# Optimization experiments

Hardware: AMD Instinct MI355X
Metric: run time of the kernel (lower is better)

## Reference

```python
import jax, jax.numpy as jnp
import numpy as np

EMB = 1024
FF = 4096
NE = 8
TOPK = 2
TEMP = 1.0


def setup_inputs() -> dict:
    key = jax.random.key(0)
    ks = jax.random.split(key, 8)
    s_emb = 1.0 / np.sqrt(EMB)
    s_ff = 1.0 / np.sqrt(FF)
    x = jax.random.normal(ks[0], (4, 2048, EMB), dtype=jnp.float32)
    gate_W = jax.random.uniform(ks[1], (EMB, NE), minval=-s_emb, maxval=s_emb, dtype=jnp.float32)
    gate_b = jax.random.uniform(ks[2], (NE,), minval=-s_emb, maxval=s_emb, dtype=jnp.float32)
    W1 = jax.random.uniform(ks[3], (NE, EMB, FF), minval=-s_emb, maxval=s_emb, dtype=jnp.float32)
    b1 = jax.random.uniform(ks[4], (NE, FF), minval=-s_emb, maxval=s_emb, dtype=jnp.float32)
    W2 = jax.random.uniform(ks[5], (NE, FF, EMB), minval=-s_ff, maxval=s_ff, dtype=jnp.float32)
    b2 = jax.random.uniform(ks[6], (NE, EMB), minval=-s_ff, maxval=s_ff, dtype=jnp.float32)
    return {"x": x, "gate_W": gate_W, "gate_b": gate_b, "W1": W1, "b1": b1, "W2": W2, "b2": b2}


def reference(x, gate_W, gate_b, W1, b1, W2, b2):
    B, S, D = x.shape
    xf = x.reshape(-1, D)  # [T, D]
    T = xf.shape[0]

    gate_logits = (xf @ gate_W + gate_b) / TEMP            # [T, E]
    gate_scores = jax.nn.softmax(gate_logits, axis=-1)     # [T, E]
    topk_scores, topk_idx = jax.lax.top_k(gate_scores, TOPK)
    topk_scores = topk_scores / jnp.sum(topk_scores, axis=-1, keepdims=True)

    # combine_weights[t, e] = sum_i topk_scores[t, i] * (topk_idx[t, i] == e)
    onehot = jax.nn.one_hot(topk_idx, NE, dtype=xf.dtype)  # [T, K, E]
    combine = jnp.einsum('tk,tke->te', topk_scores, onehot)  # [T, E]

    # Dense per-expert FFN (dropout is identity in eval): h = gelu(x W1 + b1); y = h W2 + b2
    h = jax.nn.gelu(jnp.einsum('td,edf->etf', xf, W1) + b1[:, None, :], approximate=False)
    y = jnp.einsum('etf,efd->etd', h, W2) + b2[:, None, :]  # [E, T, D]
    out = jnp.einsum('te,etd->td', combine, y).reshape(B, S, D)

    # Load-balance auxiliary loss
    expert_counts = jnp.sum(onehot, axis=(0, 1))            # [E]
    expert_fraction = expert_counts / (T * TOPK)
    routing_weights = jnp.mean(gate_scores, axis=0)
    aux_loss = NE * jnp.sum(expert_fraction * routing_weights)
    return out, aux_loss
```

## Files before the change

kernel.cpp:

```cpp
#include <hip/hip_runtime.h>
#include <math.h>

#define EMB 1024
#define FF  4096
#define NE  8
#define TTOK 8192

typedef __attribute__((ext_vector_type(4))) float  f32x4;
typedef __attribute__((ext_vector_type(8))) __bf16 bf16x8;

#define MAXROWS  18432

#define WS_COUNTS  0
#define WS_CURSORS 1024
#define WS_SSUM    1056
#define WS_NTILES  2080
#define WS_BASE    2084
#define WS_TILE_E  2176
#define WS_TILE_RB 2816
#define WS_TKIDX   4096
#define WS_TKW     69632
#define WS_SLOT    135168
#define WS_TOKID   200704
#define WS_ROWW    274432
#define WS_BIG2    350208

#define SZ_W1T ((size_t)NE * EMB * FF * 2)
#define SZ_W2T ((size_t)NE * EMB * FF * 2)
#define SZ_XB  ((size_t)TTOK * EMB * 2)
#define SZ_H   ((size_t)MAXROWS * FF * 2)
#define SZ_Y   ((size_t)MAXROWS * EMB * 4)

__device__ inline f32x4 fzero() { f32x4 v = {0.f, 0.f, 0.f, 0.f}; return v; }

__device__ __forceinline__ void gl16(const void* g, void* l) {
    __builtin_amdgcn_global_load_lds(
        (const __attribute__((address_space(1))) void*)g,
        (__attribute__((address_space(3))) void*)l, 16, 0, 0);
}

__device__ __forceinline__ float gelu_f(float v) {
    float u = fabsf(v) * 0.70710678118654752f;
    float p = 1.0f + u * (0.278393f + u * (0.230389f + u * (0.000972f + u * 0.078108f)));
    p = p * p; p = p * p;
    float er = 1.0f - 1.0f / p;
    float s = (v >= 0.0f) ? er : -er;
    return 0.5f * v * (1.0f + s);
}

__global__ __launch_bounds__(256) void gate_kernel(
    const float* __restrict__ x, const float* __restrict__ gW, const float* __restrict__ gb,
    int* counts, float* ssum, int* tk_idx, float* tk_w)
{
    int wave = threadIdx.x >> 6;
    int lane = threadIdx.x & 63;
    int t = blockIdx.x * 4 + wave;

    float acc[NE];
#pragma unroll
    for (int e = 0; e < NE; e++) acc[e] = 0.f;

    const float* xr = x + (size_t)t * EMB;
#pragma unroll
    for (int i = 0; i < 4; i++) {
        int d0 = i * 256 + lane * 4;
        f32x4 xv = *(const f32x4*)(xr + d0);
#pragma unroll
        for (int j = 0; j < 4; j++) {
            const float* wrow = gW + (size_t)(d0 + j) * NE;
            float xs = xv[j];
#pragma unroll
            for (int e = 0; e < NE; e++) acc[e] += xs * wrow[e];
        }
    }
#pragma unroll
    for (int e = 0; e < NE; e++) {
#pragma unroll
        for (int off = 32; off; off >>= 1) acc[e] += __shfl_xor(acc[e], off, 64);
    }
    if (lane == 0) {
        float sc[NE];
        float m = -1e30f;
        for (int e = 0; e < NE; e++) { sc[e] = acc[e] + gb[e]; m = fmaxf(m, sc[e]); }
        float sum = 0.f;
        for (int e = 0; e < NE; e++) { sc[e] = expf(sc[e] - m); sum += sc[e]; }
        float inv = 1.f / sum;
        for (int e = 0; e < NE; e++) sc[e] *= inv;
        int i0 = 0; float s0 = sc[0];
        for (int e = 1; e < NE; e++) if (sc[e] > s0) { s0 = sc[e]; i0 = e; }
        int i1 = -1; float s1 = -1e30f;
        for (int e = 0; e < NE; e++) if (e != i0 && sc[e] > s1) { s1 = sc[e]; i1 = e; }
        float rn = 1.f / (s0 + s1);
        tk_idx[2 * t]     = i0;  tk_idx[2 * t + 1] = i1;
        tk_w[2 * t]       = s0 * rn;  tk_w[2 * t + 1] = s1 * rn;
        int slot = blockIdx.x & 31;
        atomicAdd(&counts[i0 * 32 + slot], 1);
        atomicAdd(&counts[i1 * 32 + slot], 1);
        for (int e = 0; e < NE; e++) atomicAdd(&ssum[e * 32 + slot], sc[e]);
    }
}

__global__ void route_build_kernel(const int* counts, const float* ssum,
                                   int* ntiles, int* base, int* tile_e, int* tile_rb,
                                   float* out_aux)
{
    if (threadIdx.x != 0 || blockIdx.x != 0) return;
    int total = 0, tiles = 0;
    float aux = 0.f;
    for (int e = 0; e < NE; e++) {
        int c = 0; float ss = 0.f;
        for (int j = 0; j < 32; j++) { c += counts[e * 32 + j]; ss += ssum[e * 32 + j]; }
        base[e] = total;
        int nt = (c + 255) >> 8;
        for (int i = 0; i < nt; i++) { tile_e[tiles] = e; tile_rb[tiles] = total + (i << 8); tiles++; }
        total += nt << 8;
        aux += ((float)c / (float)(TTOK * 2)) * (ss / (float)TTOK);
    }
    *ntiles = tiles;
    *out_aux = aux * (float)NE;
}

__global__ __launch_bounds__(256) void scatter_kernel(
    const int* __restrict__ tk_idx, const float* __restrict__ tk_w,
    const int* __restrict__ base, int* cursors, int* token_id, float* roww,
    int* slot_of)
{
    int t = blockIdx.x * 256 + threadIdx.x;
#pragma unroll
    for (int k = 0; k < 2; k++) {
        int e = tk_idx[2 * t + k];
        int pos = atomicAdd(&cursors[e], 1);
        int slot = base[e] + pos;
        token_id[slot] = t;
        roww[slot] = tk_w[2 * t + k];
        slot_of[2 * t + k] = slot;
    }
}

__global__ __launch_bounds__(256) void combine_kernel(
    const float* __restrict__ y0, const float* __restrict__ y1, int nsplit,
    const int* __restrict__ slot_of,
    const int* __restrict__ tk_idx, const float* __restrict__ tk_w,
    const float* __restrict__ b2, float* __restrict__ out)
{
    int t = blockIdx.x;
    int dq = threadIdx.x * 4;
    int s0 = slot_of[2 * t], s1 = slot_of[2 * t + 1];
    int e0 = tk_idx[2 * t], e1 = tk_idx[2 * t + 1];
    float w0 = tk_w[2 * t], w1 = tk_w[2 * t + 1];
    f32x4 ya = *(const f32x4*)(y0 + (size_t)s0 * EMB + dq);
    f32x4 yb = *(const f32x4*)(y0 + (size_t)s1 * EMB + dq);
    if (nsplit == 2) {
        f32x4 za = *(const f32x4*)(y1 + (size_t)s0 * EMB + dq);
        f32x4 zb = *(const f32x4*)(y1 + (size_t)s1 * EMB + dq);
#pragma unroll
        for (int q = 0; q < 4; q++) { ya[q] += za[q]; yb[q] += zb[q]; }
    }
    f32x4 ba = *(const f32x4*)(b2 + (size_t)e0 * EMB + dq);
    f32x4 bb = *(const f32x4*)(b2 + (size_t)e1 * EMB + dq);
    f32x4 r;
#pragma unroll
    for (int q = 0; q < 4; q++) r[q] = w0 * (ya[q] + ba[q]) + w1 * (yb[q] + bb[q]);
    *(f32x4*)(out + (size_t)t * EMB + dq) = r;
}

__global__ __launch_bounds__(256) void cvt_x_kernel(const float* __restrict__ x, __bf16* __restrict__ xb)
{
    size_t i = ((size_t)blockIdx.x * 256 + threadIdx.x) * 8;
    f32x4 a = *(const f32x4*)(x + i);
    f32x4 b = *(const f32x4*)(x + i + 4);
    bf16x8 o;
#pragma unroll
    for (int q = 0; q < 4; q++) { o[q] = (__bf16)a[q]; o[q + 4] = (__bf16)b[q]; }
    *(bf16x8*)(xb + i) = o;
}

__global__ __launch_bounds__(256) void transpose_cvt_kernel(
    const float* __restrict__ in, __bf16* __restrict__ outb, int R, int C)
{
    int e = blockIdx.z;
    const float* src = in + (size_t)e * R * C;
    __bf16* dst = outb + (size_t)e * R * C;
    __shared__ __bf16 Ls[64 * 72];
    int t = threadIdx.x;
    int r0 = blockIdx.x * 64, c0 = blockIdx.y * 64;
    int ri = t >> 4, cj = (t & 15) * 4;
#pragma unroll
    for (int p = 0; p < 4; p++) {
        int r = ri + p * 16;
        f32x4 v = *(const f32x4*)(src + (size_t)(r0 + r) * C + c0 + cj);
#pragma unroll
        for (int q = 0; q < 4; q++) Ls[(cj + q) * 72 + r] = (__bf16)v[q];
    }
    __syncthreads();
    int c = t >> 2, rq = (t & 3) * 16;
    bf16x8 a = *(bf16x8*)&Ls[c * 72 + rq];
    bf16x8 b = *(bf16x8*)&Ls[c * 72 + rq + 8];
    *(bf16x8*)(dst + (size_t)(c0 + c) * R + r0 + rq) = a;
    *(bf16x8*)(dst + (size_t)(c0 + c) * R + r0 + rq + 8) = b;
}


__device__ __forceinline__ void read_frags(const __bf16* lds, const int* off, bf16x8* v, int n) {
#pragma unroll
    for (int i = 0; i < n; i++) v[i] = *(const bf16x8*)(lds + off[i]);
}

__global__ __launch_bounds__(512, 2) void gemm1_8p(
    const __bf16* __restrict__ xb, const __bf16* __restrict__ W1T,
    const float* __restrict__ b1,
    const int* __restrict__ token_id, const int* __restrict__ tile_e,
    const int* __restrict__ tile_rb, const int* __restrict__ ntiles,
    __bf16* __restrict__ h)
{
    extern __shared__ __bf16 lds[];
    int flat = blockIdx.x;
    int c8 = flat & 7, r = flat >> 3;
    int mti = r >> 4, nb = r & 15;
    int mt = c8 * 9 + mti;
    if (mt >= *ntiles) return;
    int e = tile_e[mt], rb = tile_rb[mt];
    int n0 = nb * 256;

    int tid = threadIdx.x, lane = tid & 63, wid = tid >> 6;
    int wr = wid >> 2, wc = wid & 3;
    int cl = lane & 15, cq = lane >> 4;

    int srow = tid >> 2;
    int schunk = (tid & 3) ^ ((tid >> 3) & 3);
    const __bf16* ag[2];
#pragma unroll
    for (int hm = 0; hm < 2; hm++) {
        int tok = token_id[rb + hm * 128 + srow];
        if (tok < 0) tok = 0;
        ag[hm] = xb + (size_t)tok * EMB + schunk * 8;
    }
    const __bf16* bg[2];
#pragma unroll
    for (int hn = 0; hn < 2; hn++)
        bg[hn] = W1T + ((size_t)e * FF + (size_t)(n0 + hn * 128 + srow)) * EMB + schunk * 8;

    int sdA0 = wid * 512, sdA1 = 4096 + wid * 512;
    int sdB0 = 8192 + wid * 512, sdB1 = 12288 + wid * 512;

    int xoffe = (cq ^ ((cl >> 1) & 3)) * 8;
    int aoff[8], boff[4];
#pragma unroll
    for (int mi = 0; mi < 8; mi++) {
        int rr = wr * 128 + mi * 16 + cl;
        aoff[mi] = (rr >> 7) * 4096 + (rr & 127) * 32 + xoffe;
    }
#pragma unroll
    for (int ni = 0; ni < 4; ni++) {
        int nn = wc * 64 + ni * 16 + cl;
        boff[ni] = 8192 + (nn >> 7) * 4096 + (nn & 127) * 32 + xoffe;
    }

    f32x4 acc[8][4];
#pragma unroll
    for (int i = 0; i < 8; i++)
#pragma unroll
        for (int j = 0; j < 4; j++) acc[i][j] = fzero();

    const int NT = EMB / 32;
#pragma unroll
    for (int t0 = 0; t0 < 2; t0++) {
        __bf16* bp = lds + t0 * 16384;
        int k0 = t0 * 32;
        gl16(ag[0] + k0, bp + sdA0);
        gl16(ag[1] + k0, bp + sdA1);
        gl16(bg[0] + k0, bp + sdB0);
        gl16(bg[1] + k0, bp + sdB1);
    }
    asm volatile("s_waitcnt vmcnt(4)" ::: "memory");
    __builtin_amdgcn_s_barrier();

    int cb = 0;
#pragma unroll 1
    for (int t = 0; t < NT; t++) {
        const __bf16* cp = lds + cb * 16384;
        int sb = cb + 2; if (sb >= 3) sb -= 3;
        __bf16* sp = lds + sb * 16384;
        int kt = t + 2;
        int ko = kt * 32;
        if (kt < NT) {
            gl16(ag[0] + ko, sp + sdA0);
            gl16(ag[1] + ko, sp + sdA1);
            gl16(bg[0] + ko, sp + sdB0);
            gl16(bg[1] + ko, sp + sdB1);
        }
        bf16x8 b[4], a[8];
        read_frags(cp, boff, b, 4);
        read_frags(cp, aoff, a, 8);
        __builtin_amdgcn_s_setprio(1);
#pragma unroll
        for (int mi = 0; mi < 8; mi++)
#pragma unroll
            for (int ni = 0; ni < 4; ni++)
                acc[mi][ni] = __builtin_amdgcn_mfma_f32_16x16x32_bf16(a[mi], b[ni], acc[mi][ni], 0, 0, 0);
        __builtin_amdgcn_s_setprio(0);
        if (t < NT - 2)       { asm volatile("s_waitcnt vmcnt(4)" ::: "memory"); }
        else if (t == NT - 2) { asm volatile("s_waitcnt vmcnt(0)" ::: "memory"); }
        __builtin_amdgcn_s_barrier();
        cb = cb + 1; if (cb >= 3) cb = 0;
    }

    const float* b1g = b1 + (size_t)e * FF + n0;
#pragma unroll
    for (int mi = 0; mi < 8; mi++) {
#pragma unroll
        for (int ni = 0; ni < 4; ni++) {
            int col = wc * 64 + ni * 16 + cl;
            float bias = b1g[col];
#pragma unroll
            for (int j = 0; j < 4; j++) {
                int row = wr * 128 + mi * 16 + cq * 4 + j;
                float v = acc[mi][ni][j] + bias;
                h[(size_t)(rb + row) * FF + n0 + col] = (__bf16)gelu_f(v);
            }
        }
    }
}

__global__ __launch_bounds__(512, 2) void gemm2_8p(
    const __bf16* __restrict__ h, const __bf16* __restrict__ W2T,
    const int* __restrict__ tile_e, const int* __restrict__ tile_rb,
    const int* __restrict__ ntiles,
    float* __restrict__ y0, float* __restrict__ y1, int nsplit)
{
    extern __shared__ __bf16 lds[];
    int flat = blockIdx.x;
    int c8 = flat & 7, r = flat >> 3;
    int z = r / 36; int r36 = r - z * 36;
    int mti = r36 >> 2, nb = r36 & 3;
    int mt = c8 * 9 + mti;
    if (mt >= *ntiles) return;
    int e = tile_e[mt], rb = tile_rb[mt];
    int n0 = nb * 256;
    int KC = FF / nsplit;
    int koff = z * KC;
    float* y = z ? y1 : y0;

    int tid = threadIdx.x, lane = tid & 63, wid = tid >> 6;
    int wr = wid >> 2, wc = wid & 3;
    int cl = lane & 15, cq = lane >> 4;

    int srow = tid >> 2;
    int schunk = (tid & 3) ^ ((tid >> 3) & 3);
    const __bf16* ag[2];
#pragma unroll
    for (int hm = 0; hm < 2; hm++)
        ag[hm] = h + (size_t)(rb + hm * 128 + srow) * FF + koff + schunk * 8;
    const __bf16* bg[2];
#pragma unroll
    for (int hn = 0; hn < 2; hn++)
        bg[hn] = W2T + ((size_t)e * EMB + (size_t)(n0 + hn * 128 + srow)) * FF + koff + schunk * 8;

    int sdA0 = wid * 512, sdA1 = 4096 + wid * 512;
    int sdB0 = 8192 + wid * 512, sdB1 = 12288 + wid * 512;

    int xoffe = (cq ^ ((cl >> 1) & 3)) * 8;
    int aoff[8], boff[4];
#pragma unroll
    for (int mi = 0; mi < 8; mi++) {
        int rr = wr * 128 + mi * 16 + cl;
        aoff[mi] = (rr >> 7) * 4096 + (rr & 127) * 32 + xoffe;
    }
#pragma unroll
    for (int ni = 0; ni < 4; ni++) {
        int nn = wc * 64 + ni * 16 + cl;
        boff[ni] = 8192 + (nn >> 7) * 4096 + (nn & 127) * 32 + xoffe;
    }

    f32x4 acc[8][4];
#pragma unroll
    for (int i = 0; i < 8; i++)
#pragma unroll
        for (int j = 0; j < 4; j++) acc[i][j] = fzero();

    const int NT = KC / 32;
#pragma unroll
    for (int t0 = 0; t0 < 2; t0++) {
        __bf16* bp = lds + t0 * 16384;
        int k0 = t0 * 32;
        gl16(ag[0] + k0, bp + sdA0);
        gl16(ag[1] + k0, bp + sdA1);
        gl16(bg[0] + k0, bp + sdB0);
        gl16(bg[1] + k0, bp + sdB1);
    }
    asm volatile("s_waitcnt vmcnt(4)" ::: "memory");
    __builtin_amdgcn_s_barrier();

    int cb = 0;
#pragma unroll 1
    for (int t = 0; t < NT; t++) {
        const __bf16* cp = lds + cb * 16384;
        int sb = cb + 2; if (sb >= 3) sb -= 3;
        __bf16* sp = lds + sb * 16384;
        int kt = t + 2;
        int ko = kt * 32;
        if (kt < NT) {
            gl16(ag[0] + ko, sp + sdA0);
            gl16(ag[1] + ko, sp + sdA1);
            gl16(bg[0] + ko, sp + sdB0);
            gl16(bg[1] + ko, sp + sdB1);
        }
        bf16x8 b[4], a[8];
        read_frags(cp, boff, b, 4);
        read_frags(cp, aoff, a, 8);
        __builtin_amdgcn_s_setprio(1);
#pragma unroll
        for (int mi = 0; mi < 8; mi++)
#pragma unroll
            for (int ni = 0; ni < 4; ni++)
                acc[mi][ni] = __builtin_amdgcn_mfma_f32_16x16x32_bf16(a[mi], b[ni], acc[mi][ni], 0, 0, 0);
        __builtin_amdgcn_s_setprio(0);
        if (t < NT - 2)       { asm volatile("s_waitcnt vmcnt(4)" ::: "memory"); }
        else if (t == NT - 2) { asm volatile("s_waitcnt vmcnt(0)" ::: "memory"); }
        __builtin_amdgcn_s_barrier();
        cb = cb + 1; if (cb >= 3) cb = 0;
    }

#pragma unroll
    for (int mi = 0; mi < 8; mi++) {
#pragma unroll
        for (int ni = 0; ni < 4; ni++) {
            int col = wc * 64 + ni * 16 + cl;
#pragma unroll
            for (int j = 0; j < 4; j++) {
                int row = wr * 128 + mi * 16 + cq * 4 + j;
                y[(size_t)(rb + row) * EMB + n0 + col] = acc[mi][ni][j];
            }
        }
    }
}

extern "C" void kernel_launch(void* const* d_in, const int* in_sizes, int n_in,
                              void* d_out, int out_size, void* d_ws, size_t ws_size,
                              hipStream_t stream)
{
    const float* x   = (const float*)d_in[0];
    const float* gW  = (const float*)d_in[1];
    const float* gb  = (const float*)d_in[2];
    const float* W1  = (const float*)d_in[3];
    const float* b1  = (const float*)d_in[4];
    const float* W2  = (const float*)d_in[5];
    const float* b2  = (const float*)d_in[6];
    float* out = (float*)d_out;

    char* ws = (char*)d_ws;
    int*   counts  = (int*)(ws + WS_COUNTS);
    int*   cursors = (int*)(ws + WS_CURSORS);
    float* ssum    = (float*)(ws + WS_SSUM);
    int*   ntiles  = (int*)(ws + WS_NTILES);
    int*   base    = (int*)(ws + WS_BASE);
    int*   tile_e  = (int*)(ws + WS_TILE_E);
    int*   tile_rb = (int*)(ws + WS_TILE_RB);
    int*   tk_idx  = (int*)(ws + WS_TKIDX);
    float* tk_w    = (float*)(ws + WS_TKW);
    int*   slot_of = (int*)(ws + WS_SLOT);
    int*   token_id= (int*)(ws + WS_TOKID);
    float* roww    = (float*)(ws + WS_ROWW);

    __bf16* W1T  = (__bf16*)(ws + WS_BIG2);
    __bf16* xb   = (__bf16*)(ws + WS_BIG2 + SZ_W1T);
    __bf16* W2T  = (__bf16*)(ws + WS_BIG2 + SZ_W1T + SZ_XB);
    __bf16* hbuf = (__bf16*)(ws + WS_BIG2 + SZ_W1T + SZ_XB + SZ_W2T);
    size_t fixedend = WS_BIG2 + SZ_W1T + SZ_XB + SZ_W2T;

    float* y0 = (float*)(ws + WS_BIG2);
    float* y1 = (float*)(ws + fixedend + SZ_H);
    int nsplit = (ws_size >= fixedend + SZ_H + SZ_Y) ? 2 : 1;

    hipFuncSetAttribute((const void*)gemm1_8p, hipFuncAttributeMaxDynamicSharedMemorySize, 98304);
    hipFuncSetAttribute((const void*)gemm2_8p, hipFuncAttributeMaxDynamicSharedMemorySize, 98304);

    hipMemsetAsync(ws + WS_COUNTS, 0, 2080, stream);
    hipMemsetAsync(ws + WS_TOKID, 0xFF, (size_t)MAXROWS * 4, stream);

    cvt_x_kernel<<<TTOK * EMB / 2048, 256, 0, stream>>>(x, xb);
    transpose_cvt_kernel<<<dim3(EMB / 64, FF / 64, NE), 256, 0, stream>>>(W1, W1T, EMB, FF);
    transpose_cvt_kernel<<<dim3(FF / 64, EMB / 64, NE), 256, 0, stream>>>(W2, W2T, FF, EMB);

    gate_kernel<<<TTOK / 4, 256, 0, stream>>>(x, gW, gb, counts, ssum, tk_idx, tk_w);
    route_build_kernel<<<1, 64, 0, stream>>>(counts, ssum, ntiles, base, tile_e, tile_rb,
                                             out + (size_t)TTOK * EMB);
    scatter_kernel<<<TTOK / 256, 256, 0, stream>>>(tk_idx, tk_w, base, cursors, token_id, roww, slot_of);

    gemm1_8p<<<8 * 9 * 16, 512, 98304, stream>>>(
        xb, W1T, b1, token_id, tile_e, tile_rb, ntiles, hbuf);
    gemm2_8p<<<8 * 9 * 4 * nsplit, 512, 98304, stream>>>(
        hbuf, W2T, tile_e, tile_rb, ntiles, y0, y1, nsplit);
    combine_kernel<<<TTOK, 256, 0, stream>>>(y0, y1, nsplit, slot_of, tk_idx, tk_w, b2, out);
}
```

Measured before the change: 711.5 us.

## Deepen GEMM LDS pipeline to four stages with immediate-offset fragment reads

Both expert GEMM kernels move from a three-buffer LDS ring with prefetch distance two to a four-buffer ring with prefetch distance three. Dynamic shared memory rises from 96KB to 128KB per block. Fragment reads now use inline ds_read_b128 with immediate offsets from a single base address, and they are issued before the next global-to-LDS prefetch. A lgkmcnt wait and a sched_barrier pin the order before the MFMA block, and the final loop barrier is dropped. The aim is to hide more global-load latency and cut address arithmetic, at the cost of more LDS per block and a more rigid, hand-ordered instruction schedule.

```diff
diff --git a/kernel.cpp b/kernel.cpp
--- a/kernel.cpp
+++ b/kernel.cpp
@@ -38,6 +38,9 @@
         (const __attribute__((address_space(1))) void*)g,
         (__attribute__((address_space(3))) void*)l, 16, 0, 0);
 }
+
+#define DSR(dst, addr, off) \
+    asm volatile("ds_read_b128 %0, %1 offset:" #off : "=v"(dst) : "v"(addr))
 
 __device__ __forceinline__ float gelu_f(float v) {
     float u = fabsf(v) * 0.70710678118654752f;
@@ -201,11 +204,6 @@
 }
 
 
-__device__ __forceinline__ void read_frags(const __bf16* lds, const int* off, bf16x8* v, int n) {
-#pragma unroll
-    for (int i = 0; i < n; i++) v[i] = *(const bf16x8*)(lds + off[i]);
-}
-
 __global__ __launch_bounds__(512, 2) void gemm1_8p(
     const __bf16* __restrict__ xb, const __bf16* __restrict__ W1T,
     const float* __restrict__ b1,
@@ -243,18 +241,10 @@
     int sdA0 = wid * 512, sdA1 = 4096 + wid * 512;
     int sdB0 = 8192 + wid * 512, sdB1 = 12288 + wid * 512;
 
+    uint32_t lb = (uint32_t)(uintptr_t)(__attribute__((address_space(3))) __bf16*)lds;
     int xoffe = (cq ^ ((cl >> 1) & 3)) * 8;
-    int aoff[8], boff[4];
-#pragma unroll
-    for (int mi = 0; mi < 8; mi++) {
-        int rr = wr * 128 + mi * 16 + cl;
-        aoff[mi] = (rr >> 7) * 4096 + (rr & 127) * 32 + xoffe;
-    }
-#pragma unroll
-    for (int ni = 0; ni < 4; ni++) {
-        int nn = wc * 64 + ni * 16 + cl;
-        boff[ni] = 8192 + (nn >> 7) * 4096 + (nn & 127) * 32 + xoffe;
-    }
+    uint32_t ab0 = lb + 2u * (uint32_t)(wr * 4096 + cl * 32 + xoffe);
+    uint32_t bb0 = lb + 2u * (uint32_t)(8192 + (wc >> 1) * 4096 + ((wc & 1) * 64 + cl) * 32 + xoffe);
 
     f32x4 acc[8][4];
 #pragma unroll
@@ -264,7 +254,7 @@
 
     const int NT = EMB / 32;
 #pragma unroll
-    for (int t0 = 0; t0 < 2; t0++) {
+    for (int t0 = 0; t0 < 3; t0++) {
         __bf16* bp = lds + t0 * 16384;
         int k0 = t0 * 32;
         gl16(ag[0] + k0, bp + sdA0);
@@ -272,26 +262,33 @@
         gl16(bg[0] + k0, bp + sdB0);
         gl16(bg[1] + k0, bp + sdB1);
     }
-    asm volatile("s_waitcnt vmcnt(4)" ::: "memory");
+    asm volatile("s_waitcnt vmcnt(8)" ::: "memory");
     __builtin_amdgcn_s_barrier();
 
-    int cb = 0;
 #pragma unroll 1
     for (int t = 0; t < NT; t++) {
-        const __bf16* cp = lds + cb * 16384;
-        int sb = cb + 2; if (sb >= 3) sb -= 3;
-        __bf16* sp = lds + sb * 16384;
-        int kt = t + 2;
-        int ko = kt * 32;
+        uint32_t cboff = (uint32_t)(t & 3) * 32768u;
+        uint32_t aaddr = ab0 + cboff, baddr = bb0 + cboff;
+        bf16x8 b[4], a[8];
+        DSR(b[0], baddr, 0);    DSR(b[1], baddr, 1024);
+        DSR(b[2], baddr, 2048); DSR(b[3], baddr, 3072);
+        DSR(a[0], aaddr, 0);    DSR(a[1], aaddr, 1024);
+        DSR(a[2], aaddr, 2048); DSR(a[3], aaddr, 3072);
+        DSR(a[4], aaddr, 4096); DSR(a[5], aaddr, 5120);
+        DSR(a[6], aaddr, 6144); DSR(a[7], aaddr, 7168);
+
+        int kt = t + 3;
         if (kt < NT) {
+            __bf16* sp = lds + (kt & 3) * 16384;
+            int ko = kt * 32;
             gl16(ag[0] + ko, sp + sdA0);
             gl16(ag[1] + ko, sp + sdA1);
             gl16(bg[0] + ko, sp + sdB0);
             gl16(bg[1] + ko, sp + sdB1);
         }
-        bf16x8 b[4], a[8];
-        read_frags(cp, boff, b, 4);
-        read_frags(cp, aoff, a, 8);
+
+        asm volatile("s_waitcnt lgkmcnt(0)" ::: "memory");
+        __builtin_amdgcn_sched_barrier(0);
         __builtin_amdgcn_s_setprio(1);
 #pragma unroll
         for (int mi = 0; mi < 8; mi++)
@@ -299,10 +296,11 @@
             for (int ni = 0; ni < 4; ni++)
                 acc[mi][ni] = __builtin_amdgcn_mfma_f32_16x16x32_bf16(a[mi], b[ni], acc[mi][ni], 0, 0, 0);
         __builtin_amdgcn_s_setprio(0);
-        if (t < NT - 2)       { asm volatile("s_waitcnt vmcnt(4)" ::: "memory"); }
+
+        if (t < NT - 3)       { asm volatile("s_waitcnt vmcnt(8)" ::: "memory"); }
+        else if (t == NT - 3) { asm volatile("s_waitcnt vmcnt(4)" ::: "memory"); }
         else if (t == NT - 2) { asm volatile("s_waitcnt vmcnt(0)" ::: "memory"); }
-        __builtin_amdgcn_s_barrier();
-        cb = cb + 1; if (cb >= 3) cb = 0;
+        if (t < NT - 1) __builtin_amdgcn_s_barrier();
     }
 
     const float* b1g = b1 + (size_t)e * FF + n0;
@@ -359,18 +357,10 @@
     int sdA0 = wid * 512, sdA1 = 4096 + wid * 512;
     int sdB0 = 8192 + wid * 512, sdB1 = 12288 + wid * 512;
 
+    uint32_t lb = (uint32_t)(uintptr_t)(__attribute__((address_space(3))) __bf16*)lds;
     int xoffe = (cq ^ ((cl >> 1) & 3)) * 8;
-    int aoff[8], boff[4];
-#pragma unroll
-    for (int mi = 0; mi < 8; mi++) {
-        int rr = wr * 128 + mi * 16 + cl;
-        aoff[mi] = (rr >> 7) * 4096 + (rr & 127) * 32 + xoffe;
-    }
-#pragma unroll
-    for (int ni = 0; ni < 4; ni++) {
-        int nn = wc * 64 + ni * 16 + cl;
-        boff[ni] = 8192 + (nn >> 7) * 4096 + (nn & 127) * 32 + xoffe;
-    }
+    uint32_t ab0 = lb + 2u * (uint32_t)(wr * 4096 + cl * 32 + xoffe);
+    uint32_t bb0 = lb + 2u * (uint32_t)(8192 + (wc >> 1) * 4096 + ((wc & 1) * 64 + cl) * 32 + xoffe);
 
     f32x4 acc[8][4];
 #pragma unroll
@@ -380,7 +370,7 @@
 
     const int NT = KC / 32;
 #pragma unroll
-    for (int t0 = 0; t0 < 2; t0++) {
+    for (int t0 = 0; t0 < 3; t0++) {
         __bf16* bp = lds + t0 * 16384;
         int k0 = t0 * 32;
         gl16(ag[0] + k0, bp + sdA0);
@@ -388,26 +378,33 @@
         gl16(bg[0] + k0, bp + sdB0);
         gl16(bg[1] + k0, bp + sdB1);
     }
-    asm volatile("s_waitcnt vmcnt(4)" ::: "memory");
+    asm volatile("s_waitcnt vmcnt(8)" ::: "memory");
     __builtin_amdgcn_s_barrier();
 
-    int cb = 0;
 #pragma unroll 1
     for (int t = 0; t < NT; t++) {
-        const __bf16* cp = lds + cb * 16384;
-        int sb = cb + 2; if (sb >= 3) sb -= 3;
-        __bf16* sp = lds + sb * 16384;
-        int kt = t + 2;
-        int ko = kt * 32;
+        uint32_t cboff = (uint32_t)(t & 3) * 32768u;
+        uint32_t aaddr = ab0 + cboff, baddr = bb0 + cboff;
+        bf16x8 b[4], a[8];
+        DSR(b[0], baddr, 0);    DSR(b[1], baddr, 1024);
+        DSR(b[2], baddr, 2048); DSR(b[3], baddr, 3072);
+        DSR(a[0], aaddr, 0);    DSR(a[1], aaddr, 1024);
+        DSR(a[2], aaddr, 2048); DSR(a[3], aaddr, 3072);
+        DSR(a[4], aaddr, 4096); DSR(a[5], aaddr, 5120);
+        DSR(a[6], aaddr, 6144); DSR(a[7], aaddr, 7168);
+
+        int kt = t + 3;
         if (kt < NT) {
+            __bf16* sp = lds + (kt & 3) * 16384;
+            int ko = kt * 32;
             gl16(ag[0] + ko, sp + sdA0);
             gl16(ag[1] + ko, sp + sdA1);
             gl16(bg[0] + ko, sp + sdB0);
             gl16(bg[1] + ko, sp + sdB1);
         }
-        bf16x8 b[4], a[8];
-        read_frags(cp, boff, b, 4);
-        read_frags(cp, aoff, a, 8);
+
+        asm volatile("s_waitcnt lgkmcnt(0)" ::: "memory");
+        __builtin_amdgcn_sched_barrier(0);
         __builtin_amdgcn_s_setprio(1);
 #pragma unroll
         for (int mi = 0; mi < 8; mi++)
@@ -415,10 +412,11 @@
             for (int ni = 0; ni < 4; ni++)
                 acc[mi][ni] = __builtin_amdgcn_mfma_f32_16x16x32_bf16(a[mi], b[ni], acc[mi][ni], 0, 0, 0);
         __builtin_amdgcn_s_setprio(0);
-        if (t < NT - 2)       { asm volatile("s_waitcnt vmcnt(4)" ::: "memory"); }
+
+        if (t < NT - 3)       { asm volatile("s_waitcnt vmcnt(8)" ::: "memory"); }
+        else if (t == NT - 3) { asm volatile("s_waitcnt vmcnt(4)" ::: "memory"); }
         else if (t == NT - 2) { asm volatile("s_waitcnt vmcnt(0)" ::: "memory"); }
-        __builtin_amdgcn_s_barrier();
-        cb = cb + 1; if (cb >= 3) cb = 0;
+        if (t < NT - 1) __builtin_amdgcn_s_barrier();
     }
 
 #pragma unroll
@@ -472,8 +470,8 @@
     float* y1 = (float*)(ws + fixedend + SZ_H);
     int nsplit = (ws_size >= fixedend + SZ_H + SZ_Y) ? 2 : 1;
 
-    hipFuncSetAttribute((const void*)gemm1_8p, hipFuncAttributeMaxDynamicSharedMemorySize, 98304);
-    hipFuncSetAttribute((const void*)gemm2_8p, hipFuncAttributeMaxDynamicSharedMemorySize, 98304);
+    hipFuncSetAttribute((const void*)gemm1_8p, hipFuncAttributeMaxDynamicSharedMemorySize, 131072);
+    hipFuncSetAttribute((const void*)gemm2_8p, hipFuncAttributeMaxDynamicSharedMemorySize, 131072);
 
     hipMemsetAsync(ws + WS_COUNTS, 0, 2080, stream);
     hipMemsetAsync(ws + WS_TOKID, 0xFF, (size_t)MAXROWS * 4, stream);
@@ -487,9 +485,9 @@
                                              out + (size_t)TTOK * EMB);
     scatter_kernel<<<TTOK / 256, 256, 0, stream>>>(tk_idx, tk_w, base, cursors, token_id, roww, slot_of);
 
-    gemm1_8p<<<8 * 9 * 16, 512, 98304, stream>>>(
+    gemm1_8p<<<8 * 9 * 16, 512, 131072, stream>>>(
         xb, W1T, b1, token_id, tile_e, tile_rb, ntiles, hbuf);
-    gemm2_8p<<<8 * 9 * 4 * nsplit, 512, 98304, stream>>>(
+    gemm2_8p<<<8 * 9 * 4 * nsplit, 512, 131072, stream>>>(
         hbuf, W2T, tile_e, tile_rb, ntiles, y0, y1, nsplit);
     combine_kernel<<<TTOK, 256, 0, stream>>>(y0, y1, nsplit, slot_of, tk_idx, tk_w, b2, out);
 }
```

New measurement: 712.4 us. Within noise of the previous version (+0.1%).
